# Performance work log

Measured on AMD Instinct MI355X. Metric: run time of the kernel, lower is better.

The kernel has to match this reference:

```python
import jax, jax.numpy as jnp
import numpy as np

C = 512
NUM_HEADS = 8
GROUPS = 32
EPS = 1e-5


def setup_inputs() -> dict:
    key = jax.random.key(0)
    ks = jax.random.split(key, 7)
    B, H, W = 8, 32, 32
    x = jax.random.normal(ks[0], (B, C, H, W), dtype=jnp.float32)
    gn_w = jnp.ones((C,), dtype=jnp.float32)
    gn_b = jnp.zeros((C,), dtype=jnp.float32)
    # 1x1 convs as dense matrices [out, in]
    qkv_w = jax.random.normal(ks[1], (3 * C, C), dtype=jnp.float32) * (1.0 / np.sqrt(C))
    qkv_b = jnp.zeros((3 * C,), dtype=jnp.float32)
    proj_w = jax.random.normal(ks[2], (C, C), dtype=jnp.float32) * (1.0 / np.sqrt(C))
    proj_b = jnp.zeros((C,), dtype=jnp.float32)
    return {"x": x, "gn_w": gn_w, "gn_b": gn_b, "qkv_w": qkv_w,
            "qkv_b": qkv_b, "proj_w": proj_w, "proj_b": proj_b}


def reference(x, gn_w, gn_b, qkv_w, qkv_b, proj_w, proj_b):
    B, Cc, H, W = x.shape
    nh = NUM_HEADS
    d = Cc // nh
    N = H * W

    # GroupNorm(32, C) with affine
    xg = x.reshape(B, GROUPS, Cc // GROUPS, H, W)
    mean = jnp.mean(xg, axis=(2, 3, 4), keepdims=True)
    var = jnp.var(xg, axis=(2, 3, 4), keepdims=True)
    hn = ((xg - mean) * jax.lax.rsqrt(var + EPS)).reshape(B, Cc, H, W)
    hn = hn * gn_w[None, :, None, None] + gn_b[None, :, None, None]

    # 1x1 conv QKV projection: [B, 3C, H, W]
    qkv = jnp.einsum('oc,bchw->bohw', qkv_w, hn) + qkv_b[None, :, None, None]
    q, k, v = jnp.split(qkv, 3, axis=1)

    def to_heads(t):  # [B, C, H, W] -> [B, nh, N, d]
        return t.reshape(B, nh, d, N).transpose(0, 1, 3, 2)

    q, k, v = to_heads(q), to_heads(k), to_heads(v)
    scale = d ** (-0.5)
    attn = jax.nn.softmax(jnp.einsum('bhnd,bhmd->bhnm', q, k) * scale, axis=-1)
    o = jnp.einsum('bhnm,bhmd->bhnd', attn, v)          # [B, nh, N, d]
    o = o.transpose(0, 1, 3, 2).reshape(B, Cc, H, W)

    # 1x1 conv output projection + residual
    o = jnp.einsum('oc,bchw->bohw', proj_w, o) + proj_b[None, :, None, None]
    return x + o
```

## Files before the change

kernel.cpp:

```cpp
#include <hip/hip_runtime.h>

typedef __bf16 bf16x8 __attribute__((ext_vector_type(8)));
typedef float f32x4 __attribute__((ext_vector_type(4)));

#define MFMA(a, b, c) __builtin_amdgcn_mfma_f32_16x16x32_bf16(a, b, c, 0, 0, 0)

#define CS 0.18033688011112042f

__device__ __forceinline__ ushort f2bf(float f) {
    __bf16 h = (__bf16)f;
    return *(ushort*)&h;
}

__device__ __forceinline__ void stage_tile64(ushort* lds, const ushort* gbase,
                                             int row_stride, int nchunks,
                                             int wave, int lane) {
    int r8 = lane >> 3;
    int cswz = ((lane & 7) ^ r8) << 4;
#pragma unroll
    for (int c = wave; c < nchunks; c += 4) {
        const char* g = (const char*)(gbase + (size_t)(c * 8 + r8) * row_stride) + cswz;
        __builtin_amdgcn_global_load_lds(
            (const __attribute__((address_space(1))) unsigned int*)g,
            (__attribute__((address_space(3))) unsigned int*)((char*)lds + c * 1024),
            16, 0, 0);
    }
}

__device__ __forceinline__ bf16x8 lds_read_row(const ushort* lds, int row, int cb) {
    return *(const bf16x8*)((const char*)lds + row * 128 + (cb ^ ((row & 7) << 4)));
}

__global__ __launch_bounds__(256) void gn_cvt_kernel(const float* __restrict__ x,
                                                     const float* __restrict__ gnw,
                                                     const float* __restrict__ gnb,
                                                     ushort* __restrict__ hnT,
                                                     const float* __restrict__ w1,
                                                     const float* __restrict__ w2,
                                                     ushort* __restrict__ o1,
                                                     ushort* __restrict__ o2) {
    if (blockIdx.x >= 256) {
        int t = (blockIdx.x - 256) * 256 + threadIdx.x;
        const int n1q = (1536 * 512) / 4;
        float4 v;
        ushort* dst;
        int idx;
        if (t < n1q) {
            v = ((const float4*)w1)[t]; dst = o1; idx = t;
        } else {
            idx = t - n1q;
            v = ((const float4*)w2)[idx]; dst = o2;
        }
        ushort4 p;
        p.x = f2bf(v.x); p.y = f2bf(v.y); p.z = f2bf(v.z); p.w = f2bf(v.w);
        ((ushort4*)dst)[idx] = p;
        return;
    }

    int b = blockIdx.x >> 5, g = blockIdx.x & 31;
    const float* xp = x + (size_t)(b * 512 + g * 16) * 1024;
    int t = threadIdx.x;

    float s = 0.f, ss = 0.f;
    const float4* xp4 = (const float4*)xp;
    for (int i = t; i < 4096; i += 256) {
        float4 v = xp4[i];
        s += (v.x + v.y) + (v.z + v.w);
        ss += (v.x * v.x + v.y * v.y) + (v.z * v.z + v.w * v.w);
    }
#pragma unroll
    for (int off = 32; off >= 1; off >>= 1) {
        s += __shfl_xor(s, off);
        ss += __shfl_xor(ss, off);
    }
    __shared__ float red[8];
    __shared__ float sw[16], sb[16];
    int wave = t >> 6;
    if ((t & 63) == 0) { red[wave] = s; red[wave + 4] = ss; }
    if (t < 16) { sw[t] = gnw[g * 16 + t]; sb[t] = gnb[g * 16 + t]; }
    __syncthreads();
    float S = red[0] + red[1] + red[2] + red[3];
    float SS = red[4] + red[5] + red[6] + red[7];
    float mean = S * (1.0f / 16384.0f);
    float var = SS * (1.0f / 16384.0f) - mean * mean;
    float rstd = rsqrtf(var + 1e-5f);

    __shared__ ushort tile[16][258];
    int cc0 = (t & 3) * 4;
    int nb = t >> 2;
    for (int chunk = 0; chunk < 4; ++chunk) {
        __syncthreads();
#pragma unroll
        for (int cc = 0; cc < 16; ++cc) {
            float v = xp[cc * 1024 + chunk * 256 + t];
            tile[cc][t] = f2bf((v - mean) * rstd * sw[cc] + sb[cc]);
        }
        __syncthreads();
        size_t rowbase = (size_t)b * 1024 + chunk * 256;
#pragma unroll
        for (int k = 0; k < 4; ++k) {
            int nl = nb + 64 * k;
            ushort4 p;
            p.x = tile[cc0 + 0][nl];
            p.y = tile[cc0 + 1][nl];
            p.z = tile[cc0 + 2][nl];
            p.w = tile[cc0 + 3][nl];
            *(ushort4*)(hnT + (rowbase + nl) * 512 + g * 16 + cc0) = p;
        }
    }
}

__global__ __launch_bounds__(256) void gemm_qkv(const ushort* __restrict__ Wb,
                                                const ushort* __restrict__ hnT,
                                                const float* __restrict__ qkvb,
                                                ushort* __restrict__ qT,
                                                ushort* __restrict__ kT,
                                                ushort* __restrict__ vb) {
    int lane = threadIdx.x & 63, wave = threadIdx.x >> 6;
    int l15 = lane & 15, lg = lane >> 4;
    int bi = blockIdx.x;
    int b = bi & 7;
    int slot = bi >> 3;
    int m0 = (slot % 12) * 128;
    int n0 = (slot / 12) * 128;
    int mw = (wave >> 1) * 64, nw = (wave & 1) * 64;
    const ushort* bb = hnT + (size_t)b * 524288;

    __shared__ ushort abuf[2][8192];
    __shared__ ushort bbuf[2][8192];

    f32x4 acc[4][4] = {};
    stage_tile64(abuf[0], Wb + (size_t)m0 * 512, 512, 16, wave, lane);
    stage_tile64(bbuf[0], bb + (size_t)n0 * 512, 512, 16, wave, lane);
    __syncthreads();
    int cur = 0;
#pragma unroll 1
    for (int t = 0; t < 8; ++t) {
        if (t < 7) {
            stage_tile64(abuf[cur ^ 1], Wb + (size_t)m0 * 512 + (t + 1) * 64, 512, 16, wave, lane);
            stage_tile64(bbuf[cur ^ 1], bb + (size_t)n0 * 512 + (t + 1) * 64, 512, 16, wave, lane);
        }
#pragma unroll
        for (int kh = 0; kh < 2; kh++) {
            bf16x8 af[4], bfr[4];
#pragma unroll
            for (int i = 0; i < 4; i++)
                af[i] = lds_read_row(abuf[cur], mw + i * 16 + l15, kh * 64 + lg * 16);
#pragma unroll
            for (int j = 0; j < 4; j++)
                bfr[j] = lds_read_row(bbuf[cur], nw + j * 16 + l15, kh * 64 + lg * 16);
#pragma unroll
            for (int i = 0; i < 4; i++)
#pragma unroll
                for (int j = 0; j < 4; j++)
                    acc[i][j] = MFMA(af[i], bfr[j], acc[i][j]);
        }
        __syncthreads();
        cur ^= 1;
    }

#pragma unroll
    for (int i = 0; i < 4; i++) {
        int ob = m0 + mw + i * 16 + lg * 4;
        float bias[4];
#pragma unroll
        for (int r = 0; r < 4; r++) bias[r] = qkvb[ob + r];
        int part = ob >> 9;
        int oo = ob & 511;
#pragma unroll
        for (int j = 0; j < 4; j++) {
            int n = n0 + nw + j * 16 + l15;
            if (part == 2) {
#pragma unroll
                for (int r = 0; r < 4; r++)
                    vb[(size_t)(b * 512 + oo + r) * 1024 + n] = f2bf(acc[i][j][r] + bias[r]);
            } else {
                ushort* dst = part ? kT : qT;
                float sc = part ? 1.0f : CS;
                int h = oo >> 6, dd = oo & 63;
                ushort4 p;
                p.x = f2bf((acc[i][j][0] + bias[0]) * sc);
                p.y = f2bf((acc[i][j][1] + bias[1]) * sc);
                p.z = f2bf((acc[i][j][2] + bias[2]) * sc);
                p.w = f2bf((acc[i][j][3] + bias[3]) * sc);
                *(ushort4*)(dst + ((size_t)((b * 8 + h) * 1024 + n)) * 64 + dd) = p;
            }
        }
    }
}

__global__ __launch_bounds__(256) void attn_kernel(const ushort* __restrict__ qT,
                                                   const ushort* __restrict__ kT,
                                                   const ushort* __restrict__ vb,
                                                   ushort* __restrict__ aoT) {
    int bi = blockIdx.x;
    int bh = ((bi >> 6) << 3) | (bi & 7);
    int q0 = ((bi >> 3) & 7) * 128;
    int b = bh >> 3, h = bh & 7;
    int lane = threadIdx.x & 63, wave = threadIdx.x >> 6;
    int l15 = lane & 15, lg = lane >> 4;
    const ushort* qp = qT + (size_t)bh * 65536;
    const ushort* kp = kT + (size_t)bh * 65536;
    const ushort* vp = vb + (size_t)bh * 65536;

    __shared__ ushort kbuf[2][4096];
    __shared__ ushort vbuf[2][4096];
    __shared__ ushort pbuf[4][2048];
    ushort* pw = pbuf[wave];

    bf16x8 vone;
#pragma unroll
    for (int e = 0; e < 8; e++) vone[e] = (__bf16)1.0f;

    bf16x8 qf[2][2];
#pragma unroll
    for (int i = 0; i < 2; i++)
#pragma unroll
        for (int kh = 0; kh < 2; kh++)
            qf[i][kh] = *(const bf16x8*)(qp + (size_t)(q0 + wave * 32 + i * 16 + l15) * 64 + kh * 32 + lg * 8);

    f32x4 oacc[2][4] = {};
    f32x4 lacc[2] = {};

    stage_tile64(kbuf[0], kp, 64, 8, wave, lane);
    stage_tile64(vbuf[0], vp, 1024, 8, wave, lane);
    __syncthreads();
    int cur = 0;

#pragma unroll 1
    for (int t = 0; t < 16; ++t) {
        if (t < 15) {
            stage_tile64(kbuf[cur ^ 1], kp + (size_t)(t + 1) * 4096, 64, 8, wave, lane);
            stage_tile64(vbuf[cur ^ 1], vp + (t + 1) * 64, 1024, 8, wave, lane);
        }
        const ushort* kb = kbuf[cur];
        const ushort* vc = vbuf[cur];

        f32x4 sacc[2][4] = {};
        __builtin_amdgcn_s_setprio(1);
#pragma unroll
        for (int kh = 0; kh < 2; kh++)
#pragma unroll
            for (int cf = 0; cf < 4; cf++) {
                bf16x8 kf = lds_read_row(kb, cf * 16 + l15, kh * 64 + lg * 16);
                sacc[0][cf] = MFMA(qf[0][kh], kf, sacc[0][cf]);
                sacc[1][cf] = MFMA(qf[1][kh], kf, sacc[1][cf]);
            }
        __builtin_amdgcn_s_setprio(0);

#pragma unroll
        for (int i = 0; i < 2; i++)
#pragma unroll
            for (int cf = 0; cf < 4; cf++)
#pragma unroll
                for (int r = 0; r < 4; r++) {
                    float p = exp2f(sacc[i][cf][r]);
                    int row = i * 16 + lg * 4 + r;
                    int cb = (cf * 16 + l15) * 2;
                    *(__bf16*)((char*)pw + row * 128 + (cb ^ ((row & 7) << 4))) = (__bf16)p;
                }

        bf16x8 vf[2][4];
#pragma unroll
        for (int ks = 0; ks < 2; ks++)
#pragma unroll
            for (int cf = 0; cf < 4; cf++)
                vf[ks][cf] = lds_read_row(vc, cf * 16 + l15, ks * 64 + lg * 16);

        __builtin_amdgcn_s_setprio(1);
#pragma unroll
        for (int i = 0; i < 2; i++)
#pragma unroll
            for (int ks = 0; ks < 2; ks++) {
                bf16x8 pf = lds_read_row(pw, i * 16 + l15, ks * 64 + lg * 16);
                lacc[i] = MFMA(pf, vone, lacc[i]);
#pragma unroll
                for (int cf = 0; cf < 4; cf++)
                    oacc[i][cf] = MFMA(pf, vf[ks][cf], oacc[i][cf]);
            }
        __builtin_amdgcn_s_setprio(0);
        __syncthreads();
        cur ^= 1;
    }

#pragma unroll
    for (int i = 0; i < 2; i++)
#pragma unroll
        for (int r = 0; r < 4; r++) {
            float inv = 1.0f / lacc[i][r];
            int n = q0 + wave * 32 + i * 16 + lg * 4 + r;
            size_t obase = ((size_t)b * 1024 + n) * 512 + h * 64;
#pragma unroll
            for (int cf = 0; cf < 4; cf++)
                aoT[obase + cf * 16 + l15] = f2bf(oacc[i][cf][r] * inv);
        }
}

__global__ __launch_bounds__(256) void gemm_proj(const ushort* __restrict__ Wb,
                                                 const ushort* __restrict__ aoT,
                                                 const float* __restrict__ projb,
                                                 const float* __restrict__ x,
                                                 float* __restrict__ out) {
    int lane = threadIdx.x & 63, wave = threadIdx.x >> 6;
    int l15 = lane & 15, lg = lane >> 4;
    int bi = blockIdx.x;
    int b = bi & 7;
    int slot = bi >> 3;
    int m0 = (slot & 3) * 128;
    int n0 = (slot >> 2) * 64;
    int mw = (wave >> 1) * 64, nw = (wave & 1) * 32;
    const ushort* bb = aoT + (size_t)b * 524288;

    __shared__ ushort abuf[2][8192];
    __shared__ ushort bbuf[2][4096];

    f32x4 acc[4][2] = {};
    stage_tile64(abuf[0], Wb + (size_t)m0 * 512, 512, 16, wave, lane);
    stage_tile64(bbuf[0], bb + (size_t)n0 * 512, 512, 8, wave, lane);
    __syncthreads();
    int cur = 0;
#pragma unroll 1
    for (int t = 0; t < 8; ++t) {
        if (t < 7) {
            stage_tile64(abuf[cur ^ 1], Wb + (size_t)m0 * 512 + (t + 1) * 64, 512, 16, wave, lane);
            stage_tile64(bbuf[cur ^ 1], bb + (size_t)n0 * 512 + (t + 1) * 64, 512, 8, wave, lane);
        }
#pragma unroll
        for (int kh = 0; kh < 2; kh++) {
            bf16x8 af[4], bfr[2];
#pragma unroll
            for (int i = 0; i < 4; i++)
                af[i] = lds_read_row(abuf[cur], mw + i * 16 + l15, kh * 64 + lg * 16);
#pragma unroll
            for (int j = 0; j < 2; j++)
                bfr[j] = lds_read_row(bbuf[cur], nw + j * 16 + l15, kh * 64 + lg * 16);
#pragma unroll
            for (int i = 0; i < 4; i++)
#pragma unroll
                for (int j = 0; j < 2; j++)
                    acc[i][j] = MFMA(af[i], bfr[j], acc[i][j]);
        }
        __syncthreads();
        cur ^= 1;
    }

#pragma unroll
    for (int i = 0; i < 4; i++) {
        int ob = m0 + mw + i * 16 + lg * 4;
        float bias[4];
#pragma unroll
        for (int r = 0; r < 4; r++) bias[r] = projb[ob + r];
#pragma unroll
        for (int j = 0; j < 2; j++) {
            int n = n0 + nw + j * 16 + l15;
#pragma unroll
            for (int r = 0; r < 4; r++) {
                size_t idx = (size_t)(b * 512 + ob + r) * 1024 + n;
                out[idx] = x[idx] + bias[r] + acc[i][j][r];
            }
        }
    }
}

extern "C" void kernel_launch(void* const* d_in, const int* in_sizes, int n_in,
                              void* d_out, int out_size, void* d_ws, size_t ws_size,
                              hipStream_t stream) {
    const float* x     = (const float*)d_in[0];
    const float* gnw   = (const float*)d_in[1];
    const float* gnb   = (const float*)d_in[2];
    const float* qkvw  = (const float*)d_in[3];
    const float* qkvb  = (const float*)d_in[4];
    const float* projw = (const float*)d_in[5];
    const float* projb = (const float*)d_in[6];
    float* out = (float*)d_out;

    char* ws = (char*)d_ws;
    ushort* hnT    = (ushort*)(ws);
    ushort* qT     = (ushort*)(ws + (size_t)(8u << 20));
    ushort* kT     = (ushort*)(ws + (size_t)(16u << 20));
    ushort* vbuf   = (ushort*)(ws + (size_t)(24u << 20));
    ushort* qkvwb  = (ushort*)(ws + (size_t)(32u << 20));
    ushort* projwb = (ushort*)(ws + (size_t)(32u << 20) + 1572864);

    gn_cvt_kernel<<<dim3(1280), dim3(256), 0, stream>>>(x, gnw, gnb, hnT,
                                                        qkvw, projw, qkvwb, projwb);
    gemm_qkv<<<dim3(768), dim3(256), 0, stream>>>(qkvwb, hnT, qkvb, qT, kT, vbuf);
    attn_kernel<<<dim3(512), dim3(256), 0, stream>>>(qT, kT, vbuf, hnT );
    gemm_proj<<<dim3(512), dim3(256), 0, stream>>>(projwb, hnT, projb, x, out);
}
```

Measured before the change: 92.58 us.

## Keep softmax probabilities in registers by transposing S MFMA and permuting V layout

The QK^T MFMA now takes its operands swapped, so each lane's S accumulator holds key-column values that can be packed straight into bf16x8 A-operand fragments for the PV MFMA. This removes the per-wave LDS round trip, both the scattered bf16 stores and the row reads of P. To match the lane-to-key mapping, the QKV kernel writes V columns in a permuted order within each 64-column tile. The cost is a coupled layout dependency between the two kernels that must stay consistent for correctness.

```diff
diff --git a/kernel.cpp b/kernel.cpp
--- a/kernel.cpp
+++ b/kernel.cpp
@@ -171,9 +171,13 @@
         for (int j = 0; j < 4; j++) {
             int n = n0 + nw + j * 16 + l15;
             if (part == 2) {
+                int L = n & 63;
+                int cf = L >> 4;
+                int s = ((cf >> 1) << 5) | (((L >> 2) & 3) << 3) | ((cf & 1) << 2) | (L & 3);
+                int np = (n & ~63) | s;
 #pragma unroll
                 for (int r = 0; r < 4; r++)
-                    vb[(size_t)(b * 512 + oo + r) * 1024 + n] = f2bf(acc[i][j][r] + bias[r]);
+                    vb[(size_t)(b * 512 + oo + r) * 1024 + np] = f2bf(acc[i][j][r] + bias[r]);
             } else {
                 ushort* dst = part ? kT : qT;
                 float sc = part ? 1.0f : CS;
@@ -205,8 +209,6 @@
 
     __shared__ ushort kbuf[2][4096];
     __shared__ ushort vbuf[2][4096];
-    __shared__ ushort pbuf[4][2048];
-    ushort* pw = pbuf[wave];
 
     bf16x8 vone;
 #pragma unroll
@@ -243,22 +245,10 @@
 #pragma unroll
             for (int cf = 0; cf < 4; cf++) {
                 bf16x8 kf = lds_read_row(kb, cf * 16 + l15, kh * 64 + lg * 16);
-                sacc[0][cf] = MFMA(qf[0][kh], kf, sacc[0][cf]);
-                sacc[1][cf] = MFMA(qf[1][kh], kf, sacc[1][cf]);
+                sacc[0][cf] = MFMA(kf, qf[0][kh], sacc[0][cf]);
+                sacc[1][cf] = MFMA(kf, qf[1][kh], sacc[1][cf]);
             }
         __builtin_amdgcn_s_setprio(0);
-
-#pragma unroll
-        for (int i = 0; i < 2; i++)
-#pragma unroll
-            for (int cf = 0; cf < 4; cf++)
-#pragma unroll
-                for (int r = 0; r < 4; r++) {
-                    float p = exp2f(sacc[i][cf][r]);
-                    int row = i * 16 + lg * 4 + r;
-                    int cb = (cf * 16 + l15) * 2;
-                    *(__bf16*)((char*)pw + row * 128 + (cb ^ ((row & 7) << 4))) = (__bf16)p;
-                }
 
         bf16x8 vf[2][4];
 #pragma unroll
@@ -267,16 +257,29 @@
             for (int cf = 0; cf < 4; cf++)
                 vf[ks][cf] = lds_read_row(vc, cf * 16 + l15, ks * 64 + lg * 16);
 
+        bf16x8 pa[2][2];
+#pragma unroll
+        for (int i = 0; i < 2; i++)
+#pragma unroll
+            for (int ks = 0; ks < 2; ks++) {
+                bf16x8 tr;
+#pragma unroll
+                for (int jhi = 0; jhi < 2; jhi++)
+#pragma unroll
+                    for (int r = 0; r < 4; r++)
+                        tr[jhi * 4 + r] = (__bf16)exp2f(sacc[i][ks * 2 + jhi][r]);
+                pa[i][ks] = tr;
+            }
+
         __builtin_amdgcn_s_setprio(1);
 #pragma unroll
         for (int i = 0; i < 2; i++)
 #pragma unroll
             for (int ks = 0; ks < 2; ks++) {
-                bf16x8 pf = lds_read_row(pw, i * 16 + l15, ks * 64 + lg * 16);
-                lacc[i] = MFMA(pf, vone, lacc[i]);
+                lacc[i] = MFMA(pa[i][ks], vone, lacc[i]);
 #pragma unroll
                 for (int cf = 0; cf < 4; cf++)
-                    oacc[i][cf] = MFMA(pf, vf[ks][cf], oacc[i][cf]);
+                    oacc[i][cf] = MFMA(pa[i][ks], vf[ks][cf], oacc[i][cf]);
             }
         __builtin_amdgcn_s_setprio(0);
         __syncthreads();
```

After: 88.13 us. 4.8% less time.
